# Performance work log

Hardware: AMD Instinct MI355X
Metric: run time of the kernel (lower is better)

Reference implementation:

```python
import jax, jax.numpy as jnp
import numpy as np

NUM_SLICE = 32


def setup_inputs() -> dict:
    key = jax.random.key(0)
    k1, k2 = jax.random.split(key)
    B, C, N = 8, 128, 65536
    inp = jax.random.normal(k1, (B, C, N, 1), dtype=jnp.float32)
    slice_idx_mat = jax.random.randint(k2, (B, N), 0, NUM_SLICE, dtype=jnp.int32)
    return {"input": inp, "slice_idx_mat": slice_idx_mat}


def reference(input, slice_idx_mat) -> jnp.ndarray:
    # Slice max-pool: for each (batch, channel, slice), max over points whose
    # slice index equals that slice. The original CUDA kernel initializes the
    # output to 0, so the result is clamped at >= 0 (empty slices -> 0).
    B, C, N, _ = input.shape
    S = NUM_SLICE
    # [B, N, C] flattened to [B*N, C] so one segment_max covers all batches.
    x = jnp.transpose(input[..., 0], (0, 2, 1)).reshape(B * N, C)
    seg = (slice_idx_mat + jnp.arange(B, dtype=slice_idx_mat.dtype)[:, None] * S).reshape(B * N)
    pooled = jax.ops.segment_max(x, seg, num_segments=B * S)  # [B*S, C]
    pooled = jnp.maximum(pooled, jnp.float32(0.0))  # init-to-zero semantics
    out = jnp.transpose(pooled.reshape(B, S, C), (0, 2, 1))[..., None]  # [B,C,S,1]
    return out
```

## Files before the change

kernel.cpp:

```cpp
#include <hip/hip_runtime.h>

#define NUM_SLICE 32

constexpr int Bc = 8;
constexpr int Cc = 128;
constexpr int Nc = 65536;

constexpr int CPB     = 8;
constexpr int CHUNK   = 8192;
constexpr int THREADS = 256;
constexpr int PTS_PER_ITER = THREADS * 4;
constexpr int NITER   = CHUNK / PTS_PER_ITER;
constexpr int ACC_LD  = 33;

__global__ __launch_bounds__(THREADS) void init_out_kernel(float* out, int n) {
    int i = blockIdx.x * blockDim.x + threadIdx.x;
    if (i < n) out[i] = 0.0f;
}

__global__ __launch_bounds__(THREADS) void slice_pool_kernel(
    const float* __restrict__ in,
    const int*   __restrict__ idx,
    unsigned int* __restrict__ out)
{
    __shared__ unsigned int acc[CPB * ACC_LD];

    const int t = threadIdx.x;
    for (int i = t; i < CPB * ACC_LD; i += THREADS) acc[i] = 0u;
    __syncthreads();

    const int chunk = blockIdx.x;
    const int cg    = blockIdx.y;
    const int b     = blockIdx.z;
    const int c0    = cg * CPB;
    const int n0    = chunk * CHUNK;

    const int4*  __restrict__ idx4   = (const int4*)(idx + (size_t)b * Nc + n0);
    const float* __restrict__ inbase = in + ((size_t)b * Cc + c0) * Nc + n0;

    #pragma unroll 2
    for (int p = 0; p < NITER; ++p) {
        const int e   = p * THREADS + t;
        const int4 iv = idx4[e];
        const int off = e * 4;
        #pragma unroll
        for (int c = 0; c < CPB; ++c) {
            const float4 v = *(const float4*)(inbase + (size_t)c * Nc + off);
            const int base = c * ACC_LD;
            atomicMax(&acc[base + iv.x], __float_as_uint(fmaxf(v.x, 0.0f)));
            atomicMax(&acc[base + iv.y], __float_as_uint(fmaxf(v.y, 0.0f)));
            atomicMax(&acc[base + iv.z], __float_as_uint(fmaxf(v.z, 0.0f)));
            atomicMax(&acc[base + iv.w], __float_as_uint(fmaxf(v.w, 0.0f)));
        }
    }
    __syncthreads();

    if (t < CPB * NUM_SLICE) {
        const int c = t >> 5;
        const int s = t & 31;
        const unsigned int v = acc[c * ACC_LD + s];
        if (v != 0u) {
            atomicMax(&out[(((size_t)b * Cc) + c0 + c) * NUM_SLICE + s], v);
        }
    }
}

extern "C" void kernel_launch(void* const* d_in, const int* in_sizes, int n_in,
                              void* d_out, int out_size, void* d_ws, size_t ws_size,
                              hipStream_t stream) {
    const float* in  = (const float*)d_in[0];
    const int*   idx = (const int*)  d_in[1];
    float* out = (float*)d_out;

    const int n_out = Bc * Cc * NUM_SLICE;
    init_out_kernel<<<(n_out + THREADS - 1) / THREADS, THREADS, 0, stream>>>(out, n_out);

    dim3 grid(Nc / CHUNK, Cc / CPB, Bc);
    slice_pool_kernel<<<grid, THREADS, 0, stream>>>(in, idx, (unsigned int*)out);
}
```

Baseline: 57.14 us.

## Restructure slice pool into per-chunk partials with workspace reduction kernel

Each block now handles a 1024-point chunk across all 128 channels, loading the slice indices once and reusing them for every channel. It keeps two replicated shared-memory accumulators, split by thread parity, to reduce atomic contention, and skips atomics for zero values. Per-chunk partial maxima are written to a workspace and combined by a second reduction kernel, which replaces the output zero-init kernel and the global atomics. This costs an extra workspace round trip and a kernel launch, and the 512-thread blocks use a larger shared-memory footprint.

```diff
diff --git a/kernel.cpp b/kernel.cpp
--- a/kernel.cpp
+++ b/kernel.cpp
@@ -6,63 +6,78 @@
 constexpr int Cc = 128;
 constexpr int Nc = 65536;
 
-constexpr int CPB     = 8;
-constexpr int CHUNK   = 8192;
-constexpr int THREADS = 256;
-constexpr int PTS_PER_ITER = THREADS * 4;
-constexpr int NITER   = CHUNK / PTS_PER_ITER;
-constexpr int ACC_LD  = 33;
+constexpr int THREADS = 512;
+constexpr int CHUNK   = 1024;
+constexpr int PPT     = CHUNK / THREADS;
+constexpr int NCHUNK  = Nc / CHUNK;
+constexpr int NREP    = 2;
+constexpr int LD      = 33;
+constexpr int OUT_PER_B = Cc * NUM_SLICE;
 
-__global__ __launch_bounds__(THREADS) void init_out_kernel(float* out, int n) {
-    int i = blockIdx.x * blockDim.x + threadIdx.x;
-    if (i < n) out[i] = 0.0f;
-}
+typedef unsigned int u32;
+typedef uint4 u32x4;
 
-__global__ __launch_bounds__(THREADS) void slice_pool_kernel(
+__global__ __launch_bounds__(THREADS) void slice_pool_partial(
     const float* __restrict__ in,
     const int*   __restrict__ idx,
-    unsigned int* __restrict__ out)
+    u32* __restrict__ ws)
 {
-    __shared__ unsigned int acc[CPB * ACC_LD];
+    __shared__ u32 acc[Cc * NREP * LD];
 
     const int t = threadIdx.x;
-    for (int i = t; i < CPB * ACC_LD; i += THREADS) acc[i] = 0u;
+    for (int i = t; i < Cc * NREP * LD; i += THREADS) acc[i] = 0u;
     __syncthreads();
 
     const int chunk = blockIdx.x;
-    const int cg    = blockIdx.y;
-    const int b     = blockIdx.z;
-    const int c0    = cg * CPB;
+    const int b     = blockIdx.y;
     const int n0    = chunk * CHUNK;
 
-    const int4*  __restrict__ idx4   = (const int4*)(idx + (size_t)b * Nc + n0);
-    const float* __restrict__ inbase = in + ((size_t)b * Cc + c0) * Nc + n0;
+    const int2 iv = *(const int2*)(idx + (size_t)b * Nc + n0 + 2 * t);
+    const int roff = (t & 1) * LD;
+    const int s0 = roff + iv.x;
+    const int s1 = roff + iv.y;
 
-    #pragma unroll 2
-    for (int p = 0; p < NITER; ++p) {
-        const int e   = p * THREADS + t;
-        const int4 iv = idx4[e];
-        const int off = e * 4;
-        #pragma unroll
-        for (int c = 0; c < CPB; ++c) {
-            const float4 v = *(const float4*)(inbase + (size_t)c * Nc + off);
-            const int base = c * ACC_LD;
-            atomicMax(&acc[base + iv.x], __float_as_uint(fmaxf(v.x, 0.0f)));
-            atomicMax(&acc[base + iv.y], __float_as_uint(fmaxf(v.y, 0.0f)));
-            atomicMax(&acc[base + iv.z], __float_as_uint(fmaxf(v.z, 0.0f)));
-            atomicMax(&acc[base + iv.w], __float_as_uint(fmaxf(v.w, 0.0f)));
-        }
+    const float* __restrict__ inb = in + (size_t)b * Cc * Nc + n0 + 2 * t;
+
+    #pragma unroll 8
+    for (int c = 0; c < Cc; ++c) {
+        const float2 v = *(const float2*)(inb + (size_t)c * Nc);
+        const u32 bx = __float_as_uint(fmaxf(v.x, 0.0f));
+        const u32 by = __float_as_uint(fmaxf(v.y, 0.0f));
+        const int base = c * (NREP * LD);
+        if (bx) atomicMax(&acc[base + s0], bx);
+        if (by) atomicMax(&acc[base + s1], by);
     }
     __syncthreads();
 
-    if (t < CPB * NUM_SLICE) {
-        const int c = t >> 5;
-        const int s = t & 31;
-        const unsigned int v = acc[c * ACC_LD + s];
-        if (v != 0u) {
-            atomicMax(&out[(((size_t)b * Cc) + c0 + c) * NUM_SLICE + s], v);
-        }
+    u32* __restrict__ wsb = ws + ((size_t)chunk * Bc + b) * OUT_PER_B;
+    for (int i = t; i < OUT_PER_B; i += THREADS) {
+        const int c = i >> 5, s = i & 31;
+        const u32 v0 = acc[(c * NREP + 0) * LD + s];
+        const u32 v1 = acc[(c * NREP + 1) * LD + s];
+        wsb[i] = v0 > v1 ? v0 : v1;
     }
+}
+
+__global__ __launch_bounds__(256) void slice_pool_reduce(
+    const u32* __restrict__ ws,
+    u32* __restrict__ out)
+{
+    const int gid = blockIdx.x * blockDim.x + threadIdx.x;
+    const int b  = gid >> 10;
+    const int i4 = gid & 1023;
+
+    const u32x4* __restrict__ w4 = (const u32x4*)ws;
+    u32x4 m = {0u, 0u, 0u, 0u};
+    #pragma unroll 16
+    for (int chunk = 0; chunk < NCHUNK; ++chunk) {
+        const u32x4 v = w4[((size_t)chunk * Bc + b) * (OUT_PER_B / 4) + i4];
+        m.x = v.x > m.x ? v.x : m.x;
+        m.y = v.y > m.y ? v.y : m.y;
+        m.z = v.z > m.z ? v.z : m.z;
+        m.w = v.w > m.w ? v.w : m.w;
+    }
+    ((u32x4*)out)[(size_t)b * (OUT_PER_B / 4) + i4] = m;
 }
 
 extern "C" void kernel_launch(void* const* d_in, const int* in_sizes, int n_in,
@@ -70,11 +85,11 @@
                               hipStream_t stream) {
     const float* in  = (const float*)d_in[0];
     const int*   idx = (const int*)  d_in[1];
-    float* out = (float*)d_out;
+    u32* ws  = (u32*)d_ws;
+    u32* out = (u32*)d_out;
 
-    const int n_out = Bc * Cc * NUM_SLICE;
-    init_out_kernel<<<(n_out + THREADS - 1) / THREADS, THREADS, 0, stream>>>(out, n_out);
+    dim3 grid1(NCHUNK, Bc);
+    slice_pool_partial<<<grid1, THREADS, 0, stream>>>(in, idx, ws);
 
-    dim3 grid(Nc / CHUNK, Cc / CPB, Bc);
-    slice_pool_kernel<<<grid, THREADS, 0, stream>>>(in, idx, (unsigned int*)out);
+    slice_pool_reduce<<<32, 256, 0, stream>>>(ws, out);
 }
```

Result: slower. 72.48 us (+26.8%).
